# Kernel optimization log

Measured on AMD Instinct MI355X. Metric: run time of the kernel, lower is better.

The kernel has to match this reference:

```python
import jax, jax.numpy as jnp
import numpy as np

P = 16        # patch size
SIM = 0.3     # similarity threshold (forward default arg `sim`)
STY_STD = 1000.0


def patchify(imgs):
    # (N,3,H,W) -> (N, h*w, p*p*3)
    N, C, H, W = imgs.shape
    h, w = H // P, W // P
    x = imgs.reshape(N, C, h, P, w, P)
    x = jnp.einsum('nchpwq->nhwpqc', x)
    return x.reshape(N, h * w, P * P * C)


def setup_inputs() -> dict:
    key = jax.random.key(0)
    k1, k2, k3, k4 = jax.random.split(key, 4)
    N, L, D = 2, 196, 768
    x = jax.random.normal(k1, (N, L + 1, D), dtype=jnp.float32)
    imgs = jax.random.normal(k2, (N, 3, 224, 224), dtype=jnp.float32)
    # torch trunc_normal_(std=1000, a=-2, b=2) == truncated normal on [-2,2]
    learnable_sty = (jax.random.truncated_normal(
        k3, -2.0 / STY_STD, 2.0 / STY_STD, (N, L, L, 1), dtype=jnp.float32) * STY_STD)
    noise = jax.random.normal(k4, (N, L, L, 1), dtype=jnp.float32)
    return {"x": x, "imgs": imgs, "learnable_sty": learnable_sty, "noise": noise}


def reference(x, imgs, learnable_sty, noise):
    imgs = patchify(imgs)                                   # (N, L, 768)
    cls_tokens, x = x[:, :1], x[:, 1:]
    N, L, D = x.shape

    # per-patch normalization (torch.var default is unbiased -> ddof=1)
    mean = imgs.mean(axis=-1, keepdims=True)
    var = jnp.var(imgs, axis=-1, keepdims=True, ddof=1)
    imgs_n = (imgs - mean) / jnp.sqrt(var + 1e-6)
    nrm = jnp.linalg.norm(imgs_n, axis=-1)                  # (N, L)
    Sim = jnp.einsum('aik,ajk->aij', imgs_n, imgs_n) / (nrm[:, :, None] * nrm[:, None, :])

    M0 = jnp.triu((Sim > SIM).astype(jnp.float32))          # (N, L, L), binary
    rows = jnp.arange(L)

    def body(i, M):
        # original loop breaks when sum == N*L; we freeze M once that holds
        done = M.sum() == N * L
        mask = (M[:, i, :] == 0).astype(M.dtype)            # (N, L)
        # rows <= i unchanged (M*M == M for binary), rows > i masked
        upd = jnp.where(rows[None, :, None] > i, M * mask[:, None, :], M)
        return jnp.where(done, M, upd)

    M = jax.lax.fori_loop(0, L - 1, body, M0)

    # decompose: phase (con) keeps grad, amplitude (sty) is detached
    fft = jnp.fft.fftn(x, axes=(-1,))
    con, sty = jnp.angle(fft), jnp.abs(fft)
    sty_d = jax.lax.stop_gradient(sty)

    avg_sum = (M[..., None] * sty_d[:, None, :, :]).sum(axis=2)   # (N, L, D)
    sty_mask = (avg_sum > 0).astype(jnp.float32)                   # (N, L, D)
    num = M.sum(axis=2)[..., None]                                 # (N, L, 1)
    avg = avg_sum / jnp.clip(num, 1e-7, None)                      # (N, L, D)
    std = jnp.sqrt(
        (M[..., None] * (sty_d[:, None, :, :] - avg[:, :, None, :]) ** 2).sum(axis=2)
        / jnp.clip(num, 1e-7, None))                               # (N, L, D)

    sty_para = sty_mask[:, None, :, :] * learnable_sty             # (N, L, L, D)
    sty_para = sty_para / jnp.clip(sty_para.sum(axis=2, keepdims=True), 1e-7, None)
    various = noise * std[:, None, :, :] + avg[:, None, :, :]      # (N, L, L, D)
    sum_sty = (sty_para * various).sum(axis=2)                     # (N, L, D)

    # compose: ifft(amp * e^{i phase}), torch .float() keeps the real part
    out = jnp.real(jnp.fft.ifftn(sum_sty * jnp.exp(1j * con), axes=(-1,))).astype(jnp.float32)
    return jnp.concatenate((cls_tokens, out), axis=1)
```

## Files before the change

### kernel.cpp

```cpp
#include <hip/hip_runtime.h>
#include <math.h>

typedef unsigned long long u64;

#define NBATCH 2
#define LTOK 196
#define DDIM 768
#define NROWS (NBATCH*LTOK)
#define NLD (NBATCH*LTOK*DDIM)

#define PI_F 3.14159265358979323846f
#define S3 0.86602540378443864676f

#define RT 7
#define JCH 4
#define JLEN 49

__device__ __forceinline__ void fft_butterfly(float* re, float* im,
                                              const float2* T,
                                              int tau, int s, int half) {
  int sub = tau >> 7;
  int b = tau & 127;
  int j = b & (half - 1);
  int p0 = (sub << 8) + ((b >> (s - 1)) << s) + j;
  int p1 = p0 + half;
  float2 w = T[j << (8 - s)];
  float xr = re[p1], xi = im[p1];
  float tr = w.x * xr - w.y * xi;
  float ti = w.x * xi + w.y * xr;
  float ur = re[p0], ui = im[p0];
  re[p0] = ur + tr; im[p0] = ui + ti;
  re[p1] = ur - tr; im[p1] = ui - ti;
}

__device__ __forceinline__ void fft_stages(float* re, float* im,
                                           const float2* T, int t) {
#pragma unroll
  for (int s = 1; s <= 8; s++) {
    int half = 1 << (s - 1);
    fft_butterfly(re, im, T, t, s, half);
    if (t < 128) fft_butterfly(re, im, T, t + 256, s, half);
    __syncthreads();
  }
}

__global__ __launch_bounds__(256) void k_pre(const float* __restrict__ imgs,
                                             const float* __restrict__ x,
                                             float* __restrict__ u,
                                             float* __restrict__ uT,
                                             float* __restrict__ sty,
                                             float* __restrict__ phre,
                                             float* __restrict__ phim,
                                             float* __restrict__ out,
                                             unsigned int* __restrict__ counter) {
  int t = threadIdx.x;
  if (blockIdx.x >= 2 * NROWS) {
    int a = blockIdx.x - 2 * NROWS;
    if (a == 0 && t == 0) *counter = 0u;
    size_t b = (size_t)a * (LTOK + 1) * DDIM;
    out[b + t] = x[b + t];
    out[b + t + 256] = x[b + t + 256];
    out[b + t + 512] = x[b + t + 512];
    return;
  }
  if (blockIdx.x < NROWS) {
    int blk = blockIdx.x;
    int a = blk / LTOK, l = blk - a * LTOK;
    int hh = l / 14, ww = l - hh * 14;
    int p = t >> 4, q = t & 15;
    float loc[3];
    double s = 0.0, sq = 0.0;
#pragma unroll
    for (int c = 0; c < 3; c++) {
      float val = imgs[((size_t)(a * 3 + c) * 224 + (hh * 16 + p)) * 224 + (ww * 16 + q)];
      loc[c] = val;
      s += (double)val;
      sq += (double)val * (double)val;
    }
#pragma unroll
    for (int o = 32; o > 0; o >>= 1) { s += __shfl_down(s, o); sq += __shfl_down(sq, o); }
    __shared__ double rs[4], rq[4];
    __shared__ float sh_mu, sh_sc;
    if ((t & 63) == 0) { rs[t >> 6] = s; rq[t >> 6] = sq; }
    __syncthreads();
    if (t == 0) {
      double S = rs[0] + rs[1] + rs[2] + rs[3];
      double Q = rq[0] + rq[1] + rq[2] + rq[3];
      double mean = S / 768.0;
      double ss = Q - S * S / 768.0;
      if (ss < 1e-30) ss = 1e-30;
      sh_mu = (float)mean;
      sh_sc = (float)(1.0 / sqrt(ss));
    }
    __syncthreads();
    float mu = sh_mu, sc = sh_sc;
    int col = a * LTOK + l;
    size_t rbase = (size_t)col * DDIM;
#pragma unroll
    for (int c = 0; c < 3; c++) {
      int d = 3 * t + c;
      float v = (loc[c] - mu) * sc;
      u[rbase + d] = v;
      uT[(size_t)d * NROWS + col] = v;
    }
  } else {
    int blk = blockIdx.x - NROWS;
    int a = blk / LTOK, i = blk - a * LTOK;
    __shared__ float re[768], im[768];
    __shared__ float2 t256[128];
    if (t < 128) {
      float sn, cs;
      __sincosf(-2.0f * PI_F * (float)t / 256.0f, &sn, &cs);
      t256[t] = make_float2(cs, sn);
    }
    size_t row = ((size_t)a * (LTOK + 1) + 1 + i) * DDIM;
#pragma unroll
    for (int e = 0; e < 3; e++) {
      int d = t + (e << 8);
      int m = d / 3, r = d - 3 * m;
      int p = (r << 8) + (__brev((unsigned)m) >> 24);
      re[p] = x[row + d];
      im[p] = 0.f;
    }
    __syncthreads();
    fft_stages(re, im, t256, t);
    float a0r = re[t],       a0i = im[t];
    float a1r = re[256 + t], a1i = im[256 + t];
    float a2r = re[512 + t], a2i = im[512 + t];
    float sn, cs;
    __sincosf(-2.0f * PI_F * (float)t / 768.0f, &sn, &cs);
    float2 w1 = make_float2(cs, sn);
    float2 w2 = make_float2(cs * cs - sn * sn, 2.f * cs * sn);
    float b1r = a1r * w1.x - a1i * w1.y, b1i = a1r * w1.y + a1i * w1.x;
    float b2r = a2r * w2.x - a2i * w2.y, b2i = a2r * w2.y + a2i * w2.x;
    float Xr[3], Xi[3];
    Xr[0] = a0r + b1r + b2r;
    Xi[0] = a0i + b1i + b2i;
    Xr[1] = a0r + (-0.5f * b1r + S3 * b1i) + (-0.5f * b2r - S3 * b2i);
    Xi[1] = a0i + (-0.5f * b1i - S3 * b1r) + (-0.5f * b2i + S3 * b2r);
    Xr[2] = a0r + (-0.5f * b1r - S3 * b1i) + (-0.5f * b2r + S3 * b2i);
    Xi[2] = a0i + (-0.5f * b1i + S3 * b1r) + (-0.5f * b2i - S3 * b2r);
    size_t ob = ((size_t)a * LTOK + i) * DDIM + t;
#pragma unroll
    for (int s = 0; s < 3; s++) {
      float mag = sqrtf(Xr[s] * Xr[s] + Xi[s] * Xi[s]);
      size_t o = ob + (s << 8);
      sty[o] = mag;
      if (mag > 0.f) { phre[o] = Xr[s] / mag; phim[o] = Xi[s] / mag; }
      else           { phre[o] = 1.f;         phim[o] = 0.f;         }
    }
  }
}

union SimSMem {
  struct { float ui[768]; u64 mask[4]; } sim;
  struct { u64 Ml[NROWS * 4]; int red[4]; int done; } greedy;
};

__global__ __launch_bounds__(256) void k_sim(const float* __restrict__ u,
                                             const float* __restrict__ uT,
                                             u64* __restrict__ Mb,
                                             unsigned int* __restrict__ counter) {
  __shared__ SimSMem sm;
  __shared__ int s_last;
  int t = threadIdx.x;
  {
    int task = blockIdx.x;
    int a = task / LTOK, i = task - a * LTOK;
    if (t < 4) sm.sim.mask[t] = 0ull;
    size_t rbase = ((size_t)a * LTOK + i) * DDIM;
#pragma unroll
    for (int e = 0; e < 3; e++) {
      int d = t + (e << 8);
      sm.sim.ui[d] = u[rbase + d];
    }
    __syncthreads();
    int j = i + t;
    if (j < LTOK) {
      const float* col = uT + (a * LTOK + j);
      float dot = 0.f;
#pragma unroll 8
      for (int d = 0; d < 768; d++) dot += sm.sim.ui[d] * col[(size_t)d * NROWS];
      if (dot > 0.3f) atomicOr(&sm.sim.mask[j >> 6], 1ull << (j & 63));
    }
    __syncthreads();
    if (t < 4) Mb[((size_t)a * LTOK + i) * 4 + t] = sm.sim.mask[t];
  }
  __syncthreads();
  if (t == 0) {
    __threadfence();
    unsigned prev = atomicAdd(counter, 1u);
    s_last = (prev == NROWS - 1) ? 1 : 0;
  }
  __syncthreads();
  if (!s_last) return;

  __threadfence();
  for (int w = t; w < NROWS * 4; w += 256)
    sm.greedy.Ml[w] = __hip_atomic_load(&Mb[w], __ATOMIC_ACQUIRE, __HIP_MEMORY_SCOPE_AGENT);
  __syncthreads();
  for (int i = 0; i < LTOK - 1; i++) {
    int s = 0;
    for (int w = t; w < NROWS * 4; w += 256) s += __popcll(sm.greedy.Ml[w]);
#pragma unroll
    for (int o = 32; o > 0; o >>= 1) s += __shfl_down(s, o);
    if ((t & 63) == 0) sm.greedy.red[t >> 6] = s;
    __syncthreads();
    if (t == 0)
      sm.greedy.done = ((sm.greedy.red[0] + sm.greedy.red[1] +
                         sm.greedy.red[2] + sm.greedy.red[3]) == NROWS) ? 1 : 0;
    __syncthreads();
    if (sm.greedy.done) break;
    for (int w = t; w < NROWS * 4; w += 256) {
      int a = w / (LTOK * 4);
      int rem = w - a * (LTOK * 4);
      int r = rem >> 2, wi = rem & 3;
      if (r > i) sm.greedy.Ml[w] &= ~sm.greedy.Ml[(a * LTOK + i) * 4 + wi];
    }
    __syncthreads();
  }
  for (int w = t; w < NROWS * 4; w += 256) Mb[w] = sm.greedy.Ml[w];
}

__global__ __launch_bounds__(256) void k_stats(const u64* __restrict__ Mb,
                                               const float* __restrict__ sty,
                                               float* __restrict__ savg,
                                               float* __restrict__ sstd,
                                               float* __restrict__ smsk) {
  int blk = blockIdx.x;
  int a = blk / LTOK, i = blk - a * LTOK;
  __shared__ u64 mrow[4];
  int t = threadIdx.x;
  if (t < 4) mrow[t] = Mb[((size_t)a * LTOK + i) * 4 + t];
  __syncthreads();
  int num = __popcll(mrow[0]) + __popcll(mrow[1]) + __popcll(mrow[2]) + __popcll(mrow[3]);
  float fnum = fmaxf((float)num, 1e-7f);
  float acc0 = 0.f, acc1 = 0.f, acc2 = 0.f;
  for (int w = 0; w < 4; w++) {
    u64 m = mrow[w];
    while (m) {
      int b = __ffsll(m) - 1; m &= (m - 1);
      int j = (w << 6) + b;
      const float* sr = sty + ((size_t)a * LTOK + j) * DDIM;
      acc0 += sr[t]; acc1 += sr[t + 256]; acc2 += sr[t + 512];
    }
  }
  float av0 = acc0 / fnum, av1 = acc1 / fnum, av2 = acc2 / fnum;
  float sq0 = 0.f, sq1 = 0.f, sq2 = 0.f;
  for (int w = 0; w < 4; w++) {
    u64 m = mrow[w];
    while (m) {
      int b = __ffsll(m) - 1; m &= (m - 1);
      int j = (w << 6) + b;
      const float* sr = sty + ((size_t)a * LTOK + j) * DDIM;
      float d0 = sr[t] - av0, d1 = sr[t + 256] - av1, d2 = sr[t + 512] - av2;
      sq0 += d0 * d0; sq1 += d1 * d1; sq2 += d2 * d2;
    }
  }
  size_t o = ((size_t)a * LTOK + i) * DDIM + t;
  float mk0 = acc0 > 0.f ? 1.f : 0.f;
  float mk1 = acc1 > 0.f ? 1.f : 0.f;
  float mk2 = acc2 > 0.f ? 1.f : 0.f;
  smsk[o] = mk0;            smsk[o + 256] = mk1;            smsk[o + 512] = mk2;
  savg[o] = mk0 * av0;      savg[o + 256] = mk1 * av1;      savg[o + 512] = mk2 * av2;
  sstd[o] = mk0 * sqrtf(sq0 / fnum);
  sstd[o + 256] = mk1 * sqrtf(sq1 / fnum);
  sstd[o + 512] = mk2 * sqrtf(sq2 / fnum);
}

__global__ __launch_bounds__(256) void k_comb(const float* __restrict__ ls,
                                              const float* __restrict__ nz,
                                              const float* __restrict__ savg,
                                              const float* __restrict__ sstd,
                                              const float* __restrict__ smsk,
                                              float* __restrict__ numP,
                                              float* __restrict__ denP) {
  int blk = blockIdx.x;
  int a = blk / 336;
  int rem = blk - a * 336;
  int it = rem / 12;
  int r2 = rem - it * 12;
  int dc = r2 >> 2;
  int jc = r2 & 3;
  int i0 = it * RT;
  int j0 = jc * JLEN;
  int t = threadIdx.x;
  int d = (dc << 8) + t;
  __shared__ float lsr[RT][JLEN], lnr[RT][JLEN];
  for (int idx = t; idx < RT * JLEN; idx += 256) {
    int ii = idx / JLEN, j = idx - ii * JLEN;
    size_t o = ((size_t)(a * LTOK + i0 + ii)) * LTOK + j0 + j;
    float l = ls[o];
    lsr[ii][j] = l;
    lnr[ii][j] = l * nz[o];
  }
  __syncthreads();
  float nm[RT], dn[RT];
#pragma unroll
  for (int ii = 0; ii < RT; ii++) { nm[ii] = 0.f; dn[ii] = 0.f; }
#pragma unroll 7
  for (int j = 0; j < JLEN; j++) {
    size_t b = ((size_t)(a * LTOK + j0 + j)) * DDIM + d;
    float sd = sstd[b], sv = savg[b], sm = smsk[b];
#pragma unroll
    for (int ii = 0; ii < RT; ii++) {
      nm[ii] += lnr[ii][j] * sd;
      nm[ii] += lsr[ii][j] * sv;
      dn[ii] += lsr[ii][j] * sm;
    }
  }
#pragma unroll
  for (int ii = 0; ii < RT; ii++) {
    size_t o = ((size_t)jc * NROWS + (a * LTOK + i0 + ii)) * DDIM + d;
    numP[o] = nm[ii];
    denP[o] = dn[ii];
  }
}

__global__ __launch_bounds__(256) void k_ifft(const float* __restrict__ numP,
                                              const float* __restrict__ denP,
                                              const float* __restrict__ phre,
                                              const float* __restrict__ phim,
                                              float* __restrict__ out) {
  int rr = blockIdx.x;
  int t = threadIdx.x;
  int a = rr / LTOK, i = rr - a * LTOK;
  __shared__ float re[768], im[768];
  __shared__ float2 t256[128];
  if (t < 128) {
    float sn, cs;
    __sincosf(2.0f * PI_F * (float)t / 256.0f, &sn, &cs);
    t256[t] = make_float2(cs, sn);
  }
  size_t rowz = ((size_t)a * LTOK + i) * DDIM;
#pragma unroll
  for (int e = 0; e < 3; e++) {
    int d = t + (e << 8);
    float num = 0.f, den = 0.f;
#pragma unroll
    for (int jc = 0; jc < JCH; jc++) {
      size_t o = (size_t)jc * NROWS * DDIM + rowz + d;
      num += numP[o];
      den += denP[o];
    }
    float mg = num / fmaxf(den, 1e-7f);
    int m = d / 3, r = d - 3 * m;
    int p = (r << 8) + (__brev((unsigned)m) >> 24);
    re[p] = mg * phre[rowz + d];
    im[p] = mg * phim[rowz + d];
  }
  __syncthreads();
  fft_stages(re, im, t256, t);
  float a0r = re[t],       a0i = im[t];
  float a1r = re[256 + t], a1i = im[256 + t];
  float a2r = re[512 + t], a2i = im[512 + t];
  float sn, cs;
  __sincosf(2.0f * PI_F * (float)t / 768.0f, &sn, &cs);
  float2 w1 = make_float2(cs, sn);
  float2 w2 = make_float2(cs * cs - sn * sn, 2.f * cs * sn);
  float b1r = a1r * w1.x - a1i * w1.y, b1i = a1r * w1.y + a1i * w1.x;
  float b2r = a2r * w2.x - a2i * w2.y, b2i = a2r * w2.y + a2i * w2.x;
  float Xr[3];
  Xr[0] = a0r + b1r + b2r;
  Xr[1] = a0r + (-0.5f * b1r - S3 * b1i) + (-0.5f * b2r + S3 * b2i);
  Xr[2] = a0r + (-0.5f * b1r + S3 * b1i) + (-0.5f * b2r - S3 * b2i);
  size_t ob = ((size_t)a * (LTOK + 1) + 1 + i) * DDIM + t;
  const float inv = 1.0f / 768.0f;
  out[ob]       = Xr[0] * inv;
  out[ob + 256] = Xr[1] * inv;
  out[ob + 512] = Xr[2] * inv;
}

extern "C" void kernel_launch(void* const* d_in, const int* in_sizes, int n_in,
                              void* d_out, int out_size, void* d_ws, size_t ws_size,
                              hipStream_t stream) {
  (void)in_sizes; (void)n_in; (void)out_size; (void)ws_size;
  const float* x    = (const float*)d_in[0];
  const float* imgs = (const float*)d_in[1];
  const float* ls   = (const float*)d_in[2];
  const float* nz   = (const float*)d_in[3];
  float* out = (float*)d_out;

  float* wf   = (float*)d_ws;
  float* u    = wf;
  float* uT   = wf + (size_t)NLD;
  float* sty  = wf + 2 * (size_t)NLD;
  float* phre = wf + 3 * (size_t)NLD;
  float* phim = wf + 4 * (size_t)NLD;
  float* savg = wf + 5 * (size_t)NLD;
  float* sstd = wf + 6 * (size_t)NLD;
  float* smsk = wf + 7 * (size_t)NLD;
  float* numP = wf + 8 * (size_t)NLD;
  float* denP = wf + 12 * (size_t)NLD;
  u64* Mb = (u64*)(wf + 16 * (size_t)NLD);
  unsigned int* counter = (unsigned int*)(Mb + NROWS * 4);

  k_pre  <<<2 * NROWS + NBATCH, 256, 0, stream>>>(imgs, x, u, uT, sty, phre, phim, out, counter);
  k_sim  <<<NROWS, 256, 0, stream>>>(u, uT, Mb, counter);
  k_stats<<<NROWS, 256, 0, stream>>>(Mb, sty, savg, sstd, smsk);
  k_comb <<<NBATCH * 28 * 3 * JCH, 256, 0, stream>>>(ls, nz, savg, sstd, smsk, numP, denP);
  k_ifft <<<NROWS, 256, 0, stream>>>(numP, denP, phre, phim, out);
}
```

Baseline: 147.8 us.

## Replace per-row similarity dot products with tiled upper-triangular shared-memory GEMM

The similarity kernel previously launched one block per row, with each thread doing a 768-long dot product against a transposed copy of the normalized patches. It now runs a 32x32 tiled GEMM over upper-triangular tile pairs only, 28 per batch and 56 blocks total, staging float4 loads in shared memory and computing 2x2 outputs per thread. Mask bits are set with global atomicOr, so the pre-kernel now zeroes the mask buffer, and the transposed uT buffer and its strided writes are removed. This cuts redundant global reads but leaves only 56 blocks, so the GPU is lightly occupied and the serial greedy tail stays unchanged.

Result: faster. 137.9 us (-6.7%).

```diff
diff --git a/kernel.cpp b/kernel.cpp
--- a/kernel.cpp
+++ b/kernel.cpp
@@ -15,6 +15,8 @@
 #define RT 7
 #define JCH 4
 #define JLEN 49
+
+#define NSIMBLK (2 * 28)
 
 __device__ __forceinline__ void fft_butterfly(float* re, float* im,
                                               const float2* T,
@@ -47,16 +49,19 @@
 __global__ __launch_bounds__(256) void k_pre(const float* __restrict__ imgs,
                                              const float* __restrict__ x,
                                              float* __restrict__ u,
-                                             float* __restrict__ uT,
                                              float* __restrict__ sty,
                                              float* __restrict__ phre,
                                              float* __restrict__ phim,
                                              float* __restrict__ out,
+                                             u64* __restrict__ Mb,
                                              unsigned int* __restrict__ counter) {
   int t = threadIdx.x;
   if (blockIdx.x >= 2 * NROWS) {
     int a = blockIdx.x - 2 * NROWS;
-    if (a == 0 && t == 0) *counter = 0u;
+    if (a == 0) {
+      if (t == 0) *counter = 0u;
+      for (int w = t; w < NROWS * 4; w += 256) Mb[w] = 0ull;
+    }
     size_t b = (size_t)a * (LTOK + 1) * DDIM;
     out[b + t] = x[b + t];
     out[b + t + 256] = x[b + t + 256];
@@ -94,14 +99,11 @@
     }
     __syncthreads();
     float mu = sh_mu, sc = sh_sc;
-    int col = a * LTOK + l;
-    size_t rbase = (size_t)col * DDIM;
+    size_t rbase = ((size_t)(a * LTOK + l)) * DDIM;
 #pragma unroll
     for (int c = 0; c < 3; c++) {
       int d = 3 * t + c;
-      float v = (loc[c] - mu) * sc;
-      u[rbase + d] = v;
-      uT[(size_t)d * NROWS + col] = v;
+      u[rbase + d] = (loc[c] - mu) * sc;
     }
   } else {
     int blk = blockIdx.x - NROWS;
@@ -153,44 +155,69 @@
 }
 
 union SimSMem {
-  struct { float ui[768]; u64 mask[4]; } sim;
+  struct { float As[32][34]; float Bs[32][34]; } gemm;
   struct { u64 Ml[NROWS * 4]; int red[4]; int done; } greedy;
 };
 
 __global__ __launch_bounds__(256) void k_sim(const float* __restrict__ u,
-                                             const float* __restrict__ uT,
                                              u64* __restrict__ Mb,
                                              unsigned int* __restrict__ counter) {
   __shared__ SimSMem sm;
   __shared__ int s_last;
   int t = threadIdx.x;
   {
-    int task = blockIdx.x;
-    int a = task / LTOK, i = task - a * LTOK;
-    if (t < 4) sm.sim.mask[t] = 0ull;
-    size_t rbase = ((size_t)a * LTOK + i) * DDIM;
-#pragma unroll
-    for (int e = 0; e < 3; e++) {
-      int d = t + (e << 8);
-      sm.sim.ui[d] = u[rbase + d];
-    }
-    __syncthreads();
-    int j = i + t;
-    if (j < LTOK) {
-      const float* col = uT + (a * LTOK + j);
-      float dot = 0.f;
-#pragma unroll 8
-      for (int d = 0; d < 768; d++) dot += sm.sim.ui[d] * col[(size_t)d * NROWS];
-      if (dot > 0.3f) atomicOr(&sm.sim.mask[j >> 6], 1ull << (j & 63));
-    }
-    __syncthreads();
-    if (t < 4) Mb[((size_t)a * LTOK + i) * 4 + t] = sm.sim.mask[t];
+    int a = blockIdx.x / 28;
+    int p = blockIdx.x - a * 28;
+    int it = 0;
+    while (p >= 7 - it) { p -= 7 - it; it++; }
+    int jt = it + p;
+    int i0 = it << 5, j0 = jt << 5;
+    int ty = t >> 4, tx = t & 15;
+    int r = t >> 3;
+    int kq = (t & 7) << 2;
+    float c00 = 0.f, c01 = 0.f, c10 = 0.f, c11 = 0.f;
+    for (int k0 = 0; k0 < DDIM; k0 += 32) {
+      {
+        int row = i0 + r;
+        float4 v = make_float4(0.f, 0.f, 0.f, 0.f);
+        if (row < LTOK) v = *(const float4*)(u + ((size_t)(a * LTOK + row)) * DDIM + k0 + kq);
+        sm.gemm.As[kq + 0][r] = v.x; sm.gemm.As[kq + 1][r] = v.y;
+        sm.gemm.As[kq + 2][r] = v.z; sm.gemm.As[kq + 3][r] = v.w;
+      }
+      {
+        int row = j0 + r;
+        float4 v = make_float4(0.f, 0.f, 0.f, 0.f);
+        if (row < LTOK) v = *(const float4*)(u + ((size_t)(a * LTOK + row)) * DDIM + k0 + kq);
+        sm.gemm.Bs[kq + 0][r] = v.x; sm.gemm.Bs[kq + 1][r] = v.y;
+        sm.gemm.Bs[kq + 2][r] = v.z; sm.gemm.Bs[kq + 3][r] = v.w;
+      }
+      __syncthreads();
+#pragma unroll
+      for (int k = 0; k < 32; k++) {
+        float2 av = *(const float2*)&sm.gemm.As[k][ty << 1];
+        float2 bv = *(const float2*)&sm.gemm.Bs[k][tx << 1];
+        c00 += av.x * bv.x; c01 += av.x * bv.y;
+        c10 += av.y * bv.x; c11 += av.y * bv.y;
+      }
+      __syncthreads();
+    }
+    float cc[2][2] = {{c00, c01}, {c10, c11}};
+#pragma unroll
+    for (int ii = 0; ii < 2; ii++) {
+#pragma unroll
+      for (int jj = 0; jj < 2; jj++) {
+        int i = i0 + (ty << 1) + ii;
+        int j = j0 + (tx << 1) + jj;
+        if (i < LTOK && j < LTOK && j >= i && cc[ii][jj] > 0.3f)
+          atomicOr(&Mb[((size_t)(a * LTOK + i)) * 4 + (j >> 6)], 1ull << (j & 63));
+      }
+    }
   }
   __syncthreads();
   if (t == 0) {
     __threadfence();
     unsigned prev = atomicAdd(counter, 1u);
-    s_last = (prev == NROWS - 1) ? 1 : 0;
+    s_last = (prev == NSIMBLK - 1) ? 1 : 0;
   }
   __syncthreads();
   if (!s_last) return;
@@ -383,20 +410,19 @@
 
   float* wf   = (float*)d_ws;
   float* u    = wf;
-  float* uT   = wf + (size_t)NLD;
-  float* sty  = wf + 2 * (size_t)NLD;
-  float* phre = wf + 3 * (size_t)NLD;
-  float* phim = wf + 4 * (size_t)NLD;
-  float* savg = wf + 5 * (size_t)NLD;
-  float* sstd = wf + 6 * (size_t)NLD;
-  float* smsk = wf + 7 * (size_t)NLD;
-  float* numP = wf + 8 * (size_t)NLD;
-  float* denP = wf + 12 * (size_t)NLD;
-  u64* Mb = (u64*)(wf + 16 * (size_t)NLD);
+  float* sty  = wf + (size_t)NLD;
+  float* phre = wf + 2 * (size_t)NLD;
+  float* phim = wf + 3 * (size_t)NLD;
+  float* savg = wf + 4 * (size_t)NLD;
+  float* sstd = wf + 5 * (size_t)NLD;
+  float* smsk = wf + 6 * (size_t)NLD;
+  float* numP = wf + 7 * (size_t)NLD;
+  float* denP = wf + 11 * (size_t)NLD;
+  u64* Mb = (u64*)(wf + 15 * (size_t)NLD);
   unsigned int* counter = (unsigned int*)(Mb + NROWS * 4);
 
-  k_pre  <<<2 * NROWS + NBATCH, 256, 0, stream>>>(imgs, x, u, uT, sty, phre, phim, out, counter);
-  k_sim  <<<NROWS, 256, 0, stream>>>(u, uT, Mb, counter);
+  k_pre  <<<2 * NROWS + NBATCH, 256, 0, stream>>>(imgs, x, u, sty, phre, phim, out, Mb, counter);
+  k_sim  <<<NSIMBLK, 256, 0, stream>>>(u, Mb, counter);
   k_stats<<<NROWS, 256, 0, stream>>>(Mb, sty, savg, sstd, smsk);
   k_comb <<<NBATCH * 28 * 3 * JCH, 256, 0, stream>>>(ls, nz, savg, sstd, smsk, numP, denP);
   k_ifft <<<NROWS, 256, 0, stream>>>(numP, denP, phre, phim, out);
```
